# Kernel optimization log

Measured on AMD Instinct MI355X. Metric: run time of the kernel, lower is better.

## Reference

```python
import jax, jax.numpy as jnp
import numpy as np

D_MODEL = 2048
N_HEAD = 32
N_KV_HEAD = 8
N_REP = N_HEAD // N_KV_HEAD
D_K = D_MODEL // N_HEAD
THETA = 10000.0
B, S = 2, 1024


def setup_inputs() -> dict:
    key = jax.random.key(0)
    ks = jax.random.split(key, 9)
    sd = 1.0 / np.sqrt(D_MODEL)
    return {
        "x": jax.random.normal(ks[0], (B, S, D_MODEL), jnp.float32),
        "Wq": jax.random.normal(ks[1], (D_MODEL, D_MODEL), jnp.float32) * sd,
        "bq": jax.random.normal(ks[2], (D_MODEL,), jnp.float32) * 0.02,
        "Wk": jax.random.normal(ks[3], (D_MODEL, N_KV_HEAD * D_K), jnp.float32) * sd,
        "bk": jax.random.normal(ks[4], (N_KV_HEAD * D_K,), jnp.float32) * 0.02,
        "Wv": jax.random.normal(ks[5], (D_MODEL, N_KV_HEAD * D_K), jnp.float32) * sd,
        "bv": jax.random.normal(ks[6], (N_KV_HEAD * D_K,), jnp.float32) * 0.02,
        "Wo": jax.random.normal(ks[7], (D_MODEL, D_MODEL), jnp.float32) * sd,
        "bo": jax.random.normal(ks[8], (D_MODEL,), jnp.float32) * 0.02,
    }


def _apply_rope(t, pos):
    # t: [b, h, s, d_k], pos: [s]
    half = D_K // 2
    inv_freq = 1.0 / (THETA ** (jnp.arange(half, dtype=jnp.float32) * 2.0 / D_K))
    ang = pos[:, None].astype(jnp.float32) * inv_freq[None, :]  # [s, half]
    cos = jnp.cos(ang)[None, None]  # [1,1,s,half]
    sin = jnp.sin(ang)[None, None]
    te = t[..., 0::2]
    to = t[..., 1::2]
    re = te * cos - to * sin
    ro = te * sin + to * cos
    return jnp.stack([re, ro], axis=-1).reshape(t.shape)


def reference(x, Wq, bq, Wk, bk, Wv, bv, Wo, bo):
    b, s, _ = x.shape
    q = (x @ Wq + bq).reshape(b, s, N_HEAD, D_K).transpose(0, 2, 1, 3)
    k = (x @ Wk + bk).reshape(b, s, N_KV_HEAD, D_K).transpose(0, 2, 1, 3)
    v = (x @ Wv + bv).reshape(b, s, N_KV_HEAD, D_K).transpose(0, 2, 1, 3)
    pos = jnp.arange(s)
    q = _apply_rope(q, pos)
    k = _apply_rope(k, pos)
    # GQA head repeat: [b, n_kv, s, d] -> [b, n_head, s, d]
    k = jnp.repeat(k, N_REP, axis=1)
    v = jnp.repeat(v, N_REP, axis=1)
    scores = jnp.einsum('bhnd,bhmd->bhnm', q, k) / jnp.sqrt(jnp.float32(D_K))
    mask = jnp.tril(jnp.ones((s, s), dtype=bool))
    scores = jnp.where(mask[None, None], scores, jnp.float32(-jnp.inf))
    probs = jax.nn.softmax(scores, axis=-1)
    out = jnp.einsum('bhnm,bhmd->bhnd', probs, v)
    out = out.transpose(0, 2, 1, 3).reshape(b, s, D_MODEL)
    return out @ Wo + bo
```

## Files before the change

kernel.cpp:

```cpp
#include <hip/hip_runtime.h>
#include <hip/hip_bf16.h>

#define D_MODEL 2048
#define N_HEAD 32
#define N_KV_HEAD 8
#define N_REP 4
#define D_K 64
#define S_LEN 1024
#define B_SZ 2
#define M_ROWS (B_SZ * S_LEN)
#define KV_DIM (N_KV_HEAD * D_K)
#define QKV_N 3072
#define KOFF 2048
#define VOFF 2560
#define LOG2E 1.44269504088896f
#define TAB_N (S_LEN * 32)

typedef __attribute__((ext_vector_type(8))) short short8;
typedef __attribute__((ext_vector_type(4))) float f32x4;
typedef __attribute__((ext_vector_type(16))) float f32x16;

#define EXP2F(x) __builtin_amdgcn_exp2f(x)

__device__ inline unsigned short f2bf(float f) {
    union { float f; unsigned int u; } x{f};
    unsigned int r = x.u + 0x7fffu + ((x.u >> 16) & 1u);
    return (unsigned short)(r >> 16);
}
__device__ inline float bf2f(unsigned short b) {
    union { unsigned int u; float f; } x; x.u = ((unsigned int)b) << 16; return x.f;
}
__device__ inline void store_c(float* p, float v) { *p = v; }
__device__ inline void store_c(unsigned short* p, float v) { *p = f2bf(v); }

__device__ inline void load_lds16(const unsigned short* g, unsigned short* l) {
    __builtin_amdgcn_global_load_lds(
        (const __attribute__((address_space(1))) unsigned int*)g,
        (__attribute__((address_space(3))) unsigned int*)l, 16, 0, 0);
}

__device__ __forceinline__ unsigned int permpack(float hi_f, float lo_f) {
    union { float f; unsigned int u; } a{hi_f}, b{lo_f};
    return __builtin_amdgcn_perm(a.u, b.u, 0x07060302u);
}

__global__ __launch_bounds__(256) void prep_kernel(
        const float* __restrict__ x,
        const float* __restrict__ Wq_, const float* __restrict__ Wk_,
        const float* __restrict__ Wv_, const float* __restrict__ Wo_,
        const float* __restrict__ bq, const float* __restrict__ bk,
        const float* __restrict__ bv,
        unsigned short* __restrict__ xbf,
        unsigned short* __restrict__ WtQKV, unsigned short* __restrict__ WtO,
        float* __restrict__ bias_qkv, float2* __restrict__ rtab) {
    const int z = blockIdx.z;
    if (z == 6) {
        int i = (blockIdx.y * 32 + blockIdx.x) * 256 + threadIdx.x;
        if (i < QKV_N) {
            bias_qkv[i] = (i < KOFF) ? bq[i] : (i < VOFF) ? bk[i - KOFF] : bv[i - VOFF];
        }
        int j = i - QKV_N;
        if (j >= 0 && j < TAB_N) {
            int s = j >> 5, p = j & 31;
            float invf = EXP2F((float)p * -0.41524101186f);
            float ang = (float)s * invf;
            rtab[j] = make_float2(__cosf(ang), __sinf(ang));
        }
        return;
    }
    if (z >= 4) {
        int idx = ((z - 4) * 1024 + blockIdx.y * 32 + blockIdx.x) * 256 + threadIdx.x;
#pragma unroll
        for (int half = 0; half < 2; half++) {
            int i = idx + half * 524288;
            float4 v = ((const float4*)x)[i];
            unsigned int lo = (unsigned int)f2bf(v.x) | ((unsigned int)f2bf(v.y) << 16);
            unsigned int hi = (unsigned int)f2bf(v.z) | ((unsigned int)f2bf(v.w) << 16);
            ((uint2*)xbf)[i] = make_uint2(lo, hi);
        }
        return;
    }
    const float* src; unsigned short* dst; int N;
    switch (z) {
        case 0: src = Wq_; dst = WtQKV; N = D_MODEL; break;
        case 1: src = Wk_; dst = WtQKV + (size_t)KOFF * D_MODEL; N = KV_DIM; break;
        case 2: src = Wv_; dst = WtQKV + (size_t)VOFF * D_MODEL; N = KV_DIM; break;
        default: src = Wo_; dst = WtO; N = D_MODEL; break;
    }
    int n0 = blockIdx.x * 64;
    if (n0 >= N) return;
    int k0 = blockIdx.y * 64;
    int t = threadIdx.x;
    int n = n0 + (t >> 2);
    int ks = k0 + (t & 3) * 16;
    unsigned int pk[8];
#pragma unroll
    for (int i = 0; i < 8; i++) {
        float a = src[(size_t)(ks + 2 * i) * N + n];
        float b = src[(size_t)(ks + 2 * i + 1) * N + n];
        pk[i] = (unsigned int)f2bf(a) | ((unsigned int)f2bf(b) << 16);
    }
    uint4* d = (uint4*)&dst[(size_t)n * D_MODEL + ks];
    d[0] = make_uint4(pk[0], pk[1], pk[2], pk[3]);
    d[1] = make_uint4(pk[4], pk[5], pk[6], pk[7]);
}

template <typename TC, bool ROPE>
__global__ __launch_bounds__(256) void gemm_bf16_kernel(
        const unsigned short* __restrict__ A,
        const unsigned short* __restrict__ Bt,
        const float* __restrict__ bias,
        const float2* __restrict__ rtab,
        TC* __restrict__ C, int M, int N, int K) {
    __shared__ unsigned short As[2][128 * 64];
    __shared__ unsigned short Bs[2][64 * 64];
    const int tid = threadIdx.x, lane = tid & 63;
    const int w = tid >> 6, wm = w >> 1, wn = w & 1;
    const int quad = lane >> 4, lr = lane & 15;
    const int bm = blockIdx.y * 128, bn = blockIdx.x * 64;

    f32x4 acc[4][2];
#pragma unroll
    for (int i = 0; i < 4; i++)
#pragma unroll
        for (int j = 0; j < 2; j++) acc[i][j] = (f32x4){0.f, 0.f, 0.f, 0.f};

    auto stage = [&](int buf, int k0) {
#pragma unroll
        for (int it = 0; it < 4; it++) {
            int slot = it * 256 + tid;
            int row = slot >> 3;
            int qc = (slot & 7) ^ (row & 7);
            load_lds16(A + (size_t)(bm + row) * K + k0 + qc * 8, &As[buf][slot * 8]);
        }
#pragma unroll
        for (int it = 0; it < 2; it++) {
            int slot = it * 256 + tid;
            int row = slot >> 3;
            int qc = (slot & 7) ^ (row & 7);
            load_lds16(Bt + (size_t)(bn + row) * K + k0 + qc * 8, &Bs[buf][slot * 8]);
        }
    };

    stage(0, 0);
    __syncthreads();
    int cur = 0;
    for (int k0 = 0; k0 < K; k0 += 64) {
        if (k0 + 64 < K) stage(cur ^ 1, k0 + 64);
#pragma unroll
        for (int ks = 0; ks < 2; ks++) {
            short8 af[4], bf[2];
#pragma unroll
            for (int i = 0; i < 4; i++) {
                int row = wm * 64 + i * 16 + lr;
                af[i] = *(const short8*)&As[cur][(row * 8 + ((ks * 4 + quad) ^ (lr & 7))) * 8];
            }
#pragma unroll
            for (int j = 0; j < 2; j++) {
                int row = wn * 32 + j * 16 + lr;
                bf[j] = *(const short8*)&Bs[cur][(row * 8 + ((ks * 4 + quad) ^ (lr & 7))) * 8];
            }
#pragma unroll
            for (int i = 0; i < 4; i++)
#pragma unroll
                for (int j = 0; j < 2; j++)
                    acc[i][j] = __builtin_amdgcn_mfma_f32_16x16x32_bf16(af[i], bf[j], acc[i][j], 0, 0, 0);
        }
        __syncthreads();
        cur ^= 1;
    }
#pragma unroll
    for (int i = 0; i < 4; i++) {
#pragma unroll
        for (int j = 0; j < 2; j++) {
            int col = bn + wn * 32 + j * 16 + lr;
            int row0 = bm + wm * 64 + i * 16 + quad * 4;
            float bj = bias[col];
            if constexpr (ROPE) {
                bool isv = col >= VOFF;
                bool isq = col < KOFF;
                int ip = (col & 63) >> 1;
                bool even = !(lr & 1);
#pragma unroll
                for (int r = 0; r < 4; r++) {
                    float v = acc[i][j][r] + bj;
                    float pv = __shfl_xor(v, 1);
                    float outv = v;
                    if (!isv) {
                        int s = (row0 + r) & (S_LEN - 1);
                        float2 cs = rtab[s * 32 + ip];
                        outv = v * cs.x + (even ? -pv : pv) * cs.y;
                        if (isq) outv *= 0.125f * LOG2E;
                    }
                    store_c(&C[(size_t)(row0 + r) * N + col], outv);
                }
            } else {
#pragma unroll
                for (int r = 0; r < 4; r++)
                    store_c(&C[(size_t)(row0 + r) * N + col], acc[i][j][r] + bj);
            }
        }
    }
}

#define AST 72
#define RESCALE_THR 8.0f
struct Pre { uint4 k0, k1, v0, v1; };

__device__ __forceinline__ void issue_pre(const unsigned short* kb,
                                          const unsigned short* vb,
                                          int j0, int tid, Pre& p) {
    int f0 = tid, f1 = tid + 256;
    p.k0 = *(const uint4*)(kb + (size_t)(j0 + (f0 >> 3)) * QKV_N + (f0 & 7) * 8);
    p.k1 = *(const uint4*)(kb + (size_t)(j0 + (f1 >> 3)) * QKV_N + (f1 & 7) * 8);
    int kp = tid & 31, dg = tid >> 5;
    p.v0 = *(const uint4*)(vb + (size_t)(j0 + 2 * kp) * QKV_N + dg * 8);
    p.v1 = *(const uint4*)(vb + (size_t)(j0 + 2 * kp + 1) * QKV_N + dg * 8);
}
__device__ __forceinline__ void commit_pre(unsigned short* Ks, unsigned short* Vt,
                                           int tid, const Pre& p) {
    int f0 = tid, f1 = tid + 256;
    *(uint4*)&Ks[(f0 >> 3) * AST + (f0 & 7) * 8] = p.k0;
    *(uint4*)&Ks[(f1 >> 3) * AST + (f1 & 7) * 8] = p.k1;
    int kp = tid & 31, dg = tid >> 5;
    const unsigned short* ta = (const unsigned short*)&p.v0;
    const unsigned short* tb = (const unsigned short*)&p.v1;
#pragma unroll
    for (int i = 0; i < 8; i++) {
        unsigned int pk = (unsigned int)ta[i] | ((unsigned int)tb[i] << 16);
        *(unsigned int*)&Vt[(dg * 8 + i) * AST + 2 * kp] = pk;
    }
}

__global__ __launch_bounds__(256) void attn_mfma_kernel(
        const unsigned short* __restrict__ qkv,
        unsigned short* __restrict__ obf) {
    __shared__ unsigned short SM[4 * 64 * AST];
    const int tid = threadIdx.x;
    const int w = tid >> 6, lane = tid & 63;
    const int lq = lane & 31, hi = lane >> 5;
    const int hi8 = hi * 8, hi4 = hi * 4;
    const int h = blockIdx.y, b = blockIdx.z;
    const int kvh = h >> 2;
    const unsigned short* kb = qkv + (size_t)(b * S_LEN) * QKV_N + KOFF + kvh * D_K;
    const unsigned short* vb = qkv + (size_t)(b * S_LEN) * QKV_N + VOFF + kvh * D_K;

    const int qt = b ? 7 - (int)blockIdx.x : (int)blockIdx.x;
    const int nt = 2 * qt + 2;
    const int qw0 = qt * 128 + w * 32;
    const int qg = qw0 + lq;

    short8 aq[4];
    {
        const unsigned short* qp = qkv + (size_t)(b * S_LEN + qg) * QKV_N + h * D_K + hi8;
#pragma unroll
        for (int st = 0; st < 4; st++) aq[st] = *(const short8*)(qp + st * 16);
    }
    f32x16 oacc[2];
#pragma unroll
    for (int dt = 0; dt < 2; dt++)
#pragma unroll
        for (int r = 0; r < 16; r++) oacc[dt][r] = 0.f;
    float m = -1e30f, l = 0.f;

    Pre pre;
    issue_pre(kb, vb, 0, tid, pre);
    commit_pre(SM, SM + 64 * AST, tid, pre);
    if (nt > 1) issue_pre(kb, vb, 64, tid, pre);
    __syncthreads();

    for (int t = 0; t < nt; t++) {
        const int par = t & 1;
        unsigned short* Ks = SM + par * (2 * 64 * AST);
        unsigned short* Vt = Ks + 64 * AST;
        const int t64 = t * 64;
        if (t64 <= qw0 + 31) {
            f32x16 s0, s1;
#pragma unroll
            for (int r = 0; r < 16; r++) { s0[r] = 0.f; s1[r] = 0.f; }
            __builtin_amdgcn_s_setprio(1);
#pragma unroll
            for (int st = 0; st < 4; st++) {
                short8 k0 = *(const short8*)&Ks[lq * AST + st * 16 + hi8];
                short8 k1 = *(const short8*)&Ks[(32 + lq) * AST + st * 16 + hi8];
                s0 = __builtin_amdgcn_mfma_f32_32x32x16_bf16(k0, aq[st], s0, 0, 0, 0);
                s1 = __builtin_amdgcn_mfma_f32_32x32x16_bf16(k1, aq[st], s1, 0, 0, 0);
            }
            __builtin_amdgcn_s_setprio(0);
            float px[32];
#pragma unroll
            for (int r = 0; r < 16; r++) { px[r] = s0[r]; px[16 + r] = s1[r]; }
            if (t64 + 63 > qw0) {
#pragma unroll
                for (int kh = 0; kh < 2; kh++)
#pragma unroll
                    for (int r = 0; r < 16; r++) {
                        int kg = t64 + kh * 32 + ((r & 3) + 8 * (r >> 2)) + hi4;
                        if (kg > qg) px[kh * 16 + r] = -1e30f;
                    }
            }
            float tm[16];
#pragma unroll
            for (int i = 0; i < 16; i++) tm[i] = fmaxf(px[i], px[i + 16]);
#pragma unroll
            for (int i = 0; i < 8; i++) tm[i] = fmaxf(tm[i], tm[i + 8]);
#pragma unroll
            for (int i = 0; i < 4; i++) tm[i] = fmaxf(tm[i], tm[i + 4]);
            float lmax = fmaxf(fmaxf(tm[0], tm[1]), fmaxf(tm[2], tm[3]));
            union { float f; unsigned int u; } mb{lmax};
            auto rr = __builtin_amdgcn_permlane32_swap((int)mb.u, (int)mb.u, false, false);
            union { unsigned int u; float f; } ra, rb;
            ra.u = (unsigned int)rr[0];
            rb.u = (unsigned int)rr[1];
            float mn = fmaxf(m, fmaxf(ra.f, rb.f));
            if (!__all(mn - m <= RESCALE_THR)) {
                float corr = EXP2F(m - mn);
                m = mn;
                l *= corr;
#pragma unroll
                for (int dt = 0; dt < 2; dt++)
#pragma unroll
                    for (int r = 0; r < 16; r++) oacc[dt][r] *= corr;
            }
            float p[32], pm[32];
#pragma unroll
            for (int i = 0; i < 32; i++) {
                p[i] = EXP2F(px[i] - m);
                union { float f; unsigned int u; } pu{p[i]};
                pu.u &= 0xFFFF0000u;
                pm[i] = pu.f;
            }
            float ts[16];
#pragma unroll
            for (int i = 0; i < 16; i++) ts[i] = pm[i] + pm[i + 16];
#pragma unroll
            for (int i = 0; i < 8; i++) ts[i] = ts[i] + ts[i + 8];
#pragma unroll
            for (int i = 0; i < 4; i++) ts[i] = ts[i] + ts[i + 4];
            float lsum = (ts[0] + ts[1]) + (ts[2] + ts[3]);
            union { float f; unsigned int u; } sb{lsum};
            auto rr2 = __builtin_amdgcn_permlane32_swap((int)sb.u, (int)sb.u, false, false);
            union { unsigned int u; float f; } sa2, sb2;
            sa2.u = (unsigned int)rr2[0];
            sb2.u = (unsigned int)rr2[1];
            l = l + (sa2.f + sb2.f);
            short8 pf[4];
#pragma unroll
            for (int kh = 0; kh < 2; kh++)
#pragma unroll
                for (int s = 0; s < 2; s++) {
                    int base = kh * 16 + 8 * s;
                    unsigned int a01 = permpack(p[base + 1], p[base + 0]);
                    unsigned int a23 = permpack(p[base + 3], p[base + 2]);
                    unsigned int a45 = permpack(p[base + 5], p[base + 4]);
                    unsigned int a67 = permpack(p[base + 7], p[base + 6]);
                    auto r02 = __builtin_amdgcn_permlane32_swap((int)a01, (int)a45, false, false);
                    auto r13 = __builtin_amdgcn_permlane32_swap((int)a23, (int)a67, false, false);
                    union { unsigned int wd[4]; short8 v; } pk;
                    pk.wd[0] = (unsigned int)r02[0];
                    pk.wd[1] = (unsigned int)r13[0];
                    pk.wd[2] = (unsigned int)r02[1];
                    pk.wd[3] = (unsigned int)r13[1];
                    pf[kh * 2 + s] = pk.v;
                }
            __builtin_amdgcn_s_setprio(1);
#pragma unroll
            for (int dt = 0; dt < 2; dt++)
#pragma unroll
                for (int sl = 0; sl < 4; sl++) {
                    short8 va = *(const short8*)&Vt[(dt * 32 + lq) * AST + sl * 16 + hi8];
                    oacc[dt] = __builtin_amdgcn_mfma_f32_32x32x16_bf16(va, pf[sl], oacc[dt], 0, 0, 0);
                }
            __builtin_amdgcn_s_setprio(0);
        }
        if (t + 1 < nt) {
            unsigned short* Kn = SM + (par ^ 1) * (2 * 64 * AST);
            commit_pre(Kn, Kn + 64 * AST, tid, pre);
            if (t + 2 < nt) issue_pre(kb, vb, (t + 2) * 64, tid, pre);
        }
        __syncthreads();
    }
    float inv = 1.f / l;
    unsigned short* Os = SM + w * 32 * AST;
#pragma unroll
    for (int dt = 0; dt < 2; dt++)
#pragma unroll
        for (int j = 0; j < 8; j++) {
            int d = dt * 32 + ((2 * j) & 3) + 8 * (j >> 1) + hi4;
            unsigned int pk = (unsigned int)f2bf(oacc[dt][2 * j] * inv)
                            | ((unsigned int)f2bf(oacc[dt][2 * j + 1] * inv) << 16);
            *(unsigned int*)&Os[lq * AST + d] = pk;
        }
    __syncthreads();
#pragma unroll
    for (int j = 0; j < 4; j++) {
        int row = j * 8 + (lane >> 3);
        short8 v = *(const short8*)&Os[row * AST + (lane & 7) * 8];
        int qrow = b * S_LEN + qw0 + row;
        *(short8*)&obf[(size_t)qrow * D_MODEL + h * D_K + (lane & 7) * 8] = v;
    }
}

extern "C" void kernel_launch(void* const* d_in, const int* in_sizes, int n_in,
                              void* d_out, int out_size, void* d_ws, size_t ws_size,
                              hipStream_t stream) {
    const float* x  = (const float*)d_in[0];
    const float* Wq = (const float*)d_in[1];
    const float* bq = (const float*)d_in[2];
    const float* Wk = (const float*)d_in[3];
    const float* bk = (const float*)d_in[4];
    const float* Wv = (const float*)d_in[5];
    const float* bv = (const float*)d_in[6];
    const float* Wo = (const float*)d_in[7];
    const float* bo = (const float*)d_in[8];
    float* out = (float*)d_out;

    unsigned short* xbf   = (unsigned short*)d_ws;
    unsigned short* WtQKV = xbf + (size_t)M_ROWS * D_MODEL;
    unsigned short* WtO   = WtQKV + (size_t)QKV_N * D_MODEL;
    unsigned short* qkv   = WtO + (size_t)D_MODEL * D_MODEL;
    float* bias_qkv       = (float*)(qkv + (size_t)M_ROWS * QKV_N);
    float2* rtab          = (float2*)(bias_qkv + QKV_N);
    unsigned short* obf   = xbf;

    dim3 gb(256);

    prep_kernel<<<dim3(32, 32, 7), gb, 0, stream>>>(x, Wq, Wk, Wv, Wo, bq, bk, bv,
                                                    xbf, WtQKV, WtO, bias_qkv, rtab);
    gemm_bf16_kernel<unsigned short, true><<<dim3(QKV_N / 64, M_ROWS / 128), gb, 0, stream>>>(
        xbf, WtQKV, bias_qkv, rtab, qkv, M_ROWS, QKV_N, D_MODEL);
    attn_mfma_kernel<<<dim3(8, N_HEAD, B_SZ), gb, 0, stream>>>(qkv, obf);
    gemm_bf16_kernel<float, false><<<dim3(D_MODEL / 64, M_ROWS / 128), gb, 0, stream>>>(
        obf, WtO, bo, nullptr, out, M_ROWS, D_MODEL, D_MODEL);
}
```

Before: 214.4 us.

## Split GEMM K dimension across two warp groups with LDS reduction

The GEMM block grows to 512 threads, and its two 256-thread halves each handle half of the K dimension. The double-buffered LDS slots now hold one K-half each, so the prefetch overlap is gone and every iteration does sync, load and compute in sequence. The second group writes its partial accumulators to LDS, and the first group adds them before running the existing epilogue. The aim is more waves per block to hide latency, at the cost of losing the load/compute pipelining and adding a reduction step.

```diff
diff --git a/kernel.cpp b/kernel.cpp
--- a/kernel.cpp
+++ b/kernel.cpp
@@ -106,7 +106,7 @@
 }
 
 template <typename TC, bool ROPE>
-__global__ __launch_bounds__(256) void gemm_bf16_kernel(
+__global__ __launch_bounds__(512) void gemm_bf16_kernel(
         const unsigned short* __restrict__ A,
         const unsigned short* __restrict__ Bt,
         const float* __restrict__ bias,
@@ -115,9 +115,13 @@
     __shared__ unsigned short As[2][128 * 64];
     __shared__ unsigned short Bs[2][64 * 64];
     const int tid = threadIdx.x, lane = tid & 63;
-    const int w = tid >> 6, wm = w >> 1, wn = w & 1;
+    const int w = tid >> 6;
+    const int kg = w >> 2, wl = w & 3;
+    const int wm = wl >> 1, wn = wl & 1;
+    const int lt = tid & 255;
     const int quad = lane >> 4, lr = lane & 15;
     const int bm = blockIdx.y * 128, bn = blockIdx.x * 64;
+    const int kbase = kg * (K >> 1);
 
     f32x4 acc[4][2];
 #pragma unroll
@@ -125,40 +129,35 @@
 #pragma unroll
         for (int j = 0; j < 2; j++) acc[i][j] = (f32x4){0.f, 0.f, 0.f, 0.f};
 
-    auto stage = [&](int buf, int k0) {
+    for (int k0 = 0; k0 < (K >> 1); k0 += 64) {
+        __syncthreads();
 #pragma unroll
         for (int it = 0; it < 4; it++) {
-            int slot = it * 256 + tid;
+            int slot = it * 256 + lt;
             int row = slot >> 3;
             int qc = (slot & 7) ^ (row & 7);
-            load_lds16(A + (size_t)(bm + row) * K + k0 + qc * 8, &As[buf][slot * 8]);
+            load_lds16(A + (size_t)(bm + row) * K + kbase + k0 + qc * 8, &As[kg][slot * 8]);
         }
 #pragma unroll
         for (int it = 0; it < 2; it++) {
-            int slot = it * 256 + tid;
+            int slot = it * 256 + lt;
             int row = slot >> 3;
             int qc = (slot & 7) ^ (row & 7);
-            load_lds16(Bt + (size_t)(bn + row) * K + k0 + qc * 8, &Bs[buf][slot * 8]);
-        }
-    };
-
-    stage(0, 0);
-    __syncthreads();
-    int cur = 0;
-    for (int k0 = 0; k0 < K; k0 += 64) {
-        if (k0 + 64 < K) stage(cur ^ 1, k0 + 64);
+            load_lds16(Bt + (size_t)(bn + row) * K + kbase + k0 + qc * 8, &Bs[kg][slot * 8]);
+        }
+        __syncthreads();
 #pragma unroll
         for (int ks = 0; ks < 2; ks++) {
             short8 af[4], bf[2];
 #pragma unroll
             for (int i = 0; i < 4; i++) {
                 int row = wm * 64 + i * 16 + lr;
-                af[i] = *(const short8*)&As[cur][(row * 8 + ((ks * 4 + quad) ^ (lr & 7))) * 8];
+                af[i] = *(const short8*)&As[kg][(row * 8 + ((ks * 4 + quad) ^ (lr & 7))) * 8];
             }
 #pragma unroll
             for (int j = 0; j < 2; j++) {
                 int row = wn * 32 + j * 16 + lr;
-                bf[j] = *(const short8*)&Bs[cur][(row * 8 + ((ks * 4 + quad) ^ (lr & 7))) * 8];
+                bf[j] = *(const short8*)&Bs[kg][(row * 8 + ((ks * 4 + quad) ^ (lr & 7))) * 8];
             }
 #pragma unroll
             for (int i = 0; i < 4; i++)
@@ -166,9 +165,24 @@
                 for (int j = 0; j < 2; j++)
                     acc[i][j] = __builtin_amdgcn_mfma_f32_16x16x32_bf16(af[i], bf[j], acc[i][j], 0, 0, 0);
         }
-        __syncthreads();
-        cur ^= 1;
-    }
+    }
+    __syncthreads();
+    f32x4* rbuf = (f32x4*)As;
+    if (kg == 1) {
+#pragma unroll
+        for (int i = 0; i < 4; i++)
+#pragma unroll
+            for (int j = 0; j < 2; j++)
+                rbuf[(i * 2 + j) * 256 + wl * 64 + lane] = acc[i][j];
+    }
+    __syncthreads();
+    if (kg == 1) return;
+#pragma unroll
+    for (int i = 0; i < 4; i++)
+#pragma unroll
+        for (int j = 0; j < 2; j++)
+            acc[i][j] += rbuf[(i * 2 + j) * 256 + wl * 64 + lane];
+
 #pragma unroll
     for (int i = 0; i < 4; i++) {
 #pragma unroll
@@ -424,12 +438,13 @@
     unsigned short* obf   = xbf;
 
     dim3 gb(256);
+    dim3 gg(512);
 
     prep_kernel<<<dim3(32, 32, 7), gb, 0, stream>>>(x, Wq, Wk, Wv, Wo, bq, bk, bv,
                                                     xbf, WtQKV, WtO, bias_qkv, rtab);
-    gemm_bf16_kernel<unsigned short, true><<<dim3(QKV_N / 64, M_ROWS / 128), gb, 0, stream>>>(
+    gemm_bf16_kernel<unsigned short, true><<<dim3(QKV_N / 64, M_ROWS / 128), gg, 0, stream>>>(
         xbf, WtQKV, bias_qkv, rtab, qkv, M_ROWS, QKV_N, D_MODEL);
     attn_mfma_kernel<<<dim3(8, N_HEAD, B_SZ), gb, 0, stream>>>(qkv, obf);
-    gemm_bf16_kernel<float, false><<<dim3(D_MODEL / 64, M_ROWS / 128), gb, 0, stream>>>(
+    gemm_bf16_kernel<float, false><<<dim3(D_MODEL / 64, M_ROWS / 128), gg, 0, stream>>>(
         obf, WtO, bo, nullptr, out, M_ROWS, D_MODEL, D_MODEL);
 }
```

New measurement: 212.8 us, median of 2. Within noise of the previous version (-0.7%).
